# Kernel tuning notes

Hardware: AMD Instinct MI355X
Metric: run time of the kernel (lower is better)

## Reference

```python
import jax, jax.numpy as jnp
import numpy as np

H = 16  # num_heads


def setup_inputs() -> dict:
    key = jax.random.key(0)
    ks = jax.random.split(key, 12)
    B, S, D = 2, 2048, 1024
    init = lambda k, shape: (jax.random.normal(k, shape, dtype=jnp.float32) * 0.02)
    return {
        "x": jax.random.normal(ks[0], (B, S, D), dtype=jnp.float32),
        "wq": init(ks[1], (D, D)), "bq": init(ks[2], (D,)),
        "wk": init(ks[3], (D, D)), "bk": init(ks[4], (D,)),
        "wv": init(ks[5], (D, D)), "bv": init(ks[6], (D,)),
        "wo": init(ks[7], (D, D)), "bo": init(ks[8], (D,)),
        "w3d": init(ks[9], (3, D)), "b3d": init(ks[10], (3,)),
    }


def _pairwise_l2(pos):
    # pos: [B,S,3] -> [B,S,S] Euclidean distance (safe sqrt: zero grad at 0, like torch.cdist)
    sq = jnp.sum((pos[:, :, None, :] - pos[:, None, :, :]) ** 2, axis=-1)
    safe = jnp.where(sq > 0, sq, 1.0)
    return jnp.where(sq > 0, jnp.sqrt(safe), 0.0)


def reference(x, wq, bq, wk, bk, wv, bv, wo, bo, w3d, b3d):
    B, S, D = x.shape
    hd = D // H
    scale = 1.0 / (hd ** 0.5)
    # V projection -> [B,H,S,hd]  (Q/K are computed in torch forward but unused in APPROX scores)
    V = (x @ wv.T + bv).reshape(B, S, H, hd).transpose(0, 2, 1, 3)
    # 3D semantic positions and non-dot-product scores (identical across heads)
    pos = x @ w3d.T + b3d                      # [B,S,3]
    dist = _pairwise_l2(pos)                   # [B,S,S]
    scores = -dist[:, None, :, :] * scale      # [B,H,S,S] (broadcast over heads)
    causal = jnp.triu(jnp.ones((S, S), dtype=bool), k=1)
    scores = jnp.where(causal[None, None], -jnp.inf, scores)
    attn = jax.nn.softmax(scores, axis=-1)
    attn = jnp.nan_to_num(attn, nan=0.0)
    out = jnp.einsum('bhqk,bhkd->bhqd', attn, V)  # [B,H,S,hd]
    out = out.transpose(0, 2, 1, 3).reshape(B, S, D)
    return out @ wo.T + bo
```

## Files before the change

kernel.cpp:

```cpp
#include <hip/hip_runtime.h>
#include <hip/hip_bf16.h>
#include <stdint.h>


typedef __attribute__((ext_vector_type(8))) short bf16x8;
typedef __attribute__((ext_vector_type(4))) float f32x4;
typedef __attribute__((ext_vector_type(4))) unsigned short us4;

#define AS1(p) (const __attribute__((address_space(1))) unsigned int*)(p)
#define AS3(p) (__attribute__((address_space(3))) unsigned int*)(p)

__device__ __forceinline__ unsigned short f2bf(float f) {
  union { float f; unsigned u; } v; v.f = f;
  unsigned r = v.u + 0x7FFFu + ((v.u >> 16) & 1u);
  return (unsigned short)(r >> 16);
}

__global__ void k_prep(const float* __restrict__ x, const float* __restrict__ wv,
                       const float* __restrict__ wo, const float* __restrict__ bv,
                       const float* __restrict__ bo, const float* __restrict__ w3d,
                       const float* __restrict__ b3d,
                       unsigned short* __restrict__ xT, unsigned short* __restrict__ wvT,
                       unsigned short* __restrict__ wob, float* __restrict__ cvec,
                       float* __restrict__ pos) {
  __shared__ __align__(16) float lsm[64 * 68];
  const int bx = blockIdx.x, t = threadIdx.x;
  if (bx < 1024) {
    const int b = bx >> 9, rest = bx & 511, st = rest >> 4, dt = rest & 15;
    const int s0 = st * 64, d0 = dt * 64;
    const int r = t >> 2, c4 = t & 3;
    const float* src = x + (size_t)(b * 2048 + s0 + r) * 1024 + d0;
    float (*ld)[68] = (float(*)[68])lsm;
    #pragma unroll
    for (int p = 0; p < 4; p++)
      *(float4*)&ld[r][(c4 + 4 * p) * 4] = ((const float4*)src)[c4 + 4 * p];
    __syncthreads();
    #pragma unroll
    for (int p = 0; p < 4; p++) {
      const int dl = (t >> 4) + (p << 4);
      us4 o;
      #pragma unroll
      for (int k = 0; k < 4; k++)
        ((unsigned short*)&o)[k] = f2bf(ld[(t & 15) * 4 + k][dl]);
      *(us4*)(xT + ((size_t)b << 21) + (size_t)(d0 + dl) * 2048 + s0 + (t & 15) * 4) = o;
    }
  } else if (bx < 2048) {
    const int bb = bx - 1024, tr = bb >> 5, tc = bb & 31;
    const int r = t >> 5, c = t & 31;
    float (*ld)[33] = (float(*)[33])lsm;
    #pragma unroll
    for (int rr = r; rr < 32; rr += 8)
      ld[rr][c] = wv[(size_t)(tr * 32 + rr) * 1024 + tc * 32 + c];
    __syncthreads();
    #pragma unroll
    for (int rr = r; rr < 32; rr += 8)
      wvT[(size_t)(tc * 32 + rr) * 1024 + tr * 32 + c] = f2bf(ld[c][rr]);
  } else if (bx < 3072) {
    const int oo = bx - 2048;
    const float4 w = ((const float4*)(wo + (size_t)oo * 1024))[t];
    us4 ob; ob.x = f2bf(w.x); ob.y = f2bf(w.y); ob.z = f2bf(w.z); ob.w = f2bf(w.w);
    ((us4*)(wob + (size_t)oo * 1024))[t] = ob;
    const float4 b = ((const float4*)bv)[t];
    float a = w.x * b.x + w.y * b.y + w.z * b.z + w.w * b.w;
    #pragma unroll
    for (int off = 32; off; off >>= 1) a += __shfl_down(a, off, 64);
    if ((t & 63) == 0) lsm[t >> 6] = a;
    __syncthreads();
    if (t == 0) cvec[oo] = lsm[0] + lsm[1] + lsm[2] + lsm[3] + bo[oo];
  } else {
    const int row = bx - 3072;
    const float4 xv = ((const float4*)(x + (size_t)row * 1024))[t];
    const float4 w0 = ((const float4*)(w3d))[t];
    const float4 w1 = ((const float4*)(w3d + 1024))[t];
    const float4 w2 = ((const float4*)(w3d + 2048))[t];
    float a0 = xv.x*w0.x + xv.y*w0.y + xv.z*w0.z + xv.w*w0.w;
    float a1 = xv.x*w1.x + xv.y*w1.y + xv.z*w1.z + xv.w*w1.w;
    float a2 = xv.x*w2.x + xv.y*w2.y + xv.z*w2.z + xv.w*w2.w;
    #pragma unroll
    for (int off = 32; off; off >>= 1) {
      a0 += __shfl_down(a0, off, 64);
      a1 += __shfl_down(a1, off, 64);
      a2 += __shfl_down(a2, off, 64);
    }
    if ((t & 63) == 0) { lsm[(t >> 6) * 3] = a0; lsm[(t >> 6) * 3 + 1] = a1; lsm[(t >> 6) * 3 + 2] = a2; }
    __syncthreads();
    if (t == 0) {
      pos[(size_t)row*3 + 0] = lsm[0] + lsm[3] + lsm[6] + lsm[9]  + b3d[0];
      pos[(size_t)row*3 + 1] = lsm[1] + lsm[4] + lsm[7] + lsm[10] + b3d[1];
      pos[(size_t)row*3 + 2] = lsm[2] + lsm[5] + lsm[8] + lsm[11] + b3d[2];
    }
  }
}

__global__ void k_attn(const float* __restrict__ pos, unsigned short* __restrict__ Ab) {
  const int row = blockIdx.x;
  const int q = row & 2047, bb = row >> 11;
  const float* pb = pos + ((size_t)bb << 11) * 3;
  const float qx = pb[q*3], qy = pb[q*3+1], qz = pb[q*3+2];
  const float4* pb4 = (const float4*)pb;
  float v[2][4];
  float sum = 0.f;
  #pragma unroll
  for (int cc = 0; cc < 2; cc++) {
    const int j0 = (cc << 10) + (threadIdx.x << 2);
    const float4 A4 = pb4[3*(j0 >> 2)], B4 = pb4[3*(j0 >> 2) + 1], C4 = pb4[3*(j0 >> 2) + 2];
    const float px[4] = {A4.x, A4.w, B4.z, C4.y};
    const float py[4] = {A4.y, B4.x, B4.w, C4.z};
    const float pz[4] = {A4.z, B4.y, C4.x, C4.w};
    #pragma unroll
    for (int u = 0; u < 4; u++) {
      float e = 0.f;
      if (j0 + u <= q) {
        float dx = qx - px[u], dy = qy - py[u], dz = qz - pz[u];
        float sq = fmaf(dx, dx, fmaf(dy, dy, dz*dz));
        float d = sq > 0.f ? sqrtf(sq) : 0.f;
        e = __expf(-0.125f * d);
      }
      v[cc][u] = e; sum += e;
    }
  }
  #pragma unroll
  for (int off = 32; off; off >>= 1) sum += __shfl_down(sum, off, 64);
  __shared__ float red[4];
  if ((threadIdx.x & 63) == 0) red[threadIdx.x >> 6] = sum;
  __syncthreads();
  const float inv = 1.f / (red[0] + red[1] + red[2] + red[3]);
  unsigned short* orow = Ab + (size_t)row * 2048;
  #pragma unroll
  for (int cc = 0; cc < 2; cc++) {
    us4 o;
    o.x = f2bf(v[cc][0]*inv); o.y = f2bf(v[cc][1]*inv);
    o.z = f2bf(v[cc][2]*inv); o.w = f2bf(v[cc][3]*inv);
    *(us4*)(orow + (cc << 10) + (threadIdx.x << 2)) = o;
  }
}

template<int BM, int BN, int WM, int WN>
__device__ __forceinline__ void gemm_loop(
    const unsigned short* __restrict__ A, int lda,
    const unsigned short* __restrict__ Bt, int ldb,
    int m0, int n0, int kmax,
    unsigned short* lds, f32x4* acc) {
  constexpr int WAVES = WM * WN;
  constexpr int FI = BM / (WM * 16), FJ = BN / (WN * 16);
  constexpr int CPW = ((BM + BN) / 8) / WAVES;
  constexpr int BUFSZ = (BM + BN) * 64;
  const int tid = threadIdx.x, l = tid & 63, w = tid >> 6;
  const int wm = w & (WM - 1), wn = w / WM;
  const int gcol = ((l & 7) ^ (l >> 3)) << 3;

  auto stage = [&](int buf, int k0) {
    unsigned short* base = lds + buf * BUFSZ;
    #pragma unroll
    for (int e = 0; e < CPW; ++e) {
      const int c = w * CPW + e;
      const unsigned short* src;
      unsigned short* dst;
      if (c < BM / 8) {
        src = A + (size_t)(m0 + c*8 + (l >> 3)) * lda + k0 + gcol;
        dst = base + c * 512;
      } else {
        const int cb = c - BM / 8;
        src = Bt + (size_t)(n0 + cb*8 + (l >> 3)) * ldb + k0 + gcol;
        dst = base + BM * 64 + cb * 512;
      }
      __builtin_amdgcn_global_load_lds(AS1(src), AS3(dst), 16, 0, 0);
    }
  };

  auto compute = [&](int buf) {
    unsigned short* lA = lds + buf * BUFSZ;
    unsigned short* lB = lA + BM * 64;
    #pragma unroll
    for (int h = 0; h < 2; ++h) {
      const int slot = ((h << 2) | (l >> 4)) ^ (l & 7);
      bf16x8 af[FI], bfr[FJ];
      #pragma unroll
      for (int i = 0; i < FI; ++i) {
        const int ar = wm * (BM / WM) + i * 16 + (l & 15);
        af[i] = *(const bf16x8*)&lA[ar * 64 + slot * 8];
      }
      #pragma unroll
      for (int j = 0; j < FJ; ++j) {
        const int br = wn * (BN / WN) + j * 16 + (l & 15);
        bfr[j] = *(const bf16x8*)&lB[br * 64 + slot * 8];
      }
      #pragma unroll
      for (int i = 0; i < FI; ++i)
        #pragma unroll
        for (int j = 0; j < FJ; ++j)
          acc[i * FJ + j] = __builtin_amdgcn_mfma_f32_16x16x32_bf16(af[i], bfr[j], acc[i * FJ + j], 0, 0, 0);
    }
  };

  const int NT = kmax >> 6;
  stage(0, 0);
  if (NT > 1) stage(1, 64);
  int cur = 0, nxt2 = 2;
  for (int t = 0; t < NT; ++t) {
    if (t < NT - 1) {
      static_assert(CPW == 4 || CPW == 6 || CPW == 8, "vmcnt literal");
      if constexpr (CPW == 4) asm volatile("s_waitcnt vmcnt(4) lgkmcnt(0)" ::: "memory");
      else if constexpr (CPW == 6) asm volatile("s_waitcnt vmcnt(6) lgkmcnt(0)" ::: "memory");
      else asm volatile("s_waitcnt vmcnt(8) lgkmcnt(0)" ::: "memory");
    } else {
      asm volatile("s_waitcnt vmcnt(0) lgkmcnt(0)" ::: "memory");
    }
    __builtin_amdgcn_s_barrier();
    if (t + 2 < NT) stage(nxt2, (t + 2) << 6);
    compute(cur);
    cur = cur == 2 ? 0 : cur + 1;
    nxt2 = nxt2 == 2 ? 0 : nxt2 + 1;
  }
}

__global__ __launch_bounds__(256, 2) void k_gemm_axwc(
    const unsigned short* __restrict__ Ab, const unsigned short* __restrict__ xT,
    unsigned short* __restrict__ Axb,
    const unsigned short* __restrict__ wob, const unsigned short* __restrict__ wvT,
    unsigned short* __restrict__ Wcs) {
  __shared__ __align__(16) unsigned short lds[3 * (128 + 64) * 64];
  const int bx = blockIdx.x;
  const int l = threadIdx.x & 63, w = threadIdx.x >> 6;
  const int wm = w & 1, wn = w >> 1;
  if (bx < 512) {
    f32x4 acc[8] = {};
    const int b = bx >> 8;
    const int mi = b ? (bx & 15) : 15 - (bx & 15);
    const int m0 = mi * 128, n0 = ((bx >> 4) & 15) * 64;
    const unsigned short* A  = Ab + ((size_t)b << 22);
    const unsigned short* Bt = xT + ((size_t)b << 21);
    gemm_loop<128, 64, 2, 2>(A, 2048, Bt, 2048, m0, n0, m0 + 128, lds, acc);
    unsigned short* Obase = Axb + ((size_t)b << 11) * 1024;
    #pragma unroll
    for (int i = 0; i < 4; i++) {
      const int r0 = m0 + wm*64 + i*16 + ((l >> 4) << 2);
      #pragma unroll
      for (int j = 0; j < 2; j++) {
        const int cidx = n0 + wn*32 + j*16 + (l & 15);
        #pragma unroll
        for (int t = 0; t < 4; t++)
          Obase[(size_t)(r0 + t) * 1024 + cidx] = f2bf(acc[i*2 + j][t]);
      }
    }
  } else {
    f32x4 acc[4] = {};
    const int g = bx - 512;
    const int m0 = (g & 15) * 64, n0 = (g >> 4) * 64;
    gemm_loop<64, 64, 2, 2>(wob, 1024, wvT, 1024, m0, n0, 1024, lds, acc);
    #pragma unroll
    for (int i = 0; i < 2; i++) {
      const int r0 = m0 + wm*32 + i*16 + ((l >> 4) << 2);
      #pragma unroll
      for (int j = 0; j < 2; j++) {
        const int cidx = n0 + wn*32 + j*16 + (l & 15);
        #pragma unroll
        for (int t = 0; t < 4; t++)
          Wcs[(size_t)(r0 + t) * 1024 + cidx] = f2bf(acc[i*2 + j][t]);
      }
    }
  }
}

__global__ __launch_bounds__(256, 2) void k_gemm_out(
    const unsigned short* __restrict__ Axb, const unsigned short* __restrict__ Wcs,
    const float* __restrict__ cvec, float* __restrict__ out) {
  __shared__ __align__(16) unsigned short lds[3 * (128 + 64) * 64];
  f32x4 acc[8] = {};
  const int m0 = blockIdx.x * 128, n0 = blockIdx.y * 64;
  gemm_loop<128, 64, 2, 2>(Axb, 1024, Wcs, 1024, m0, n0, 1024, lds, acc);
  const int l = threadIdx.x & 63, w = threadIdx.x >> 6;
  const int wm = w & 1, wn = w >> 1;
  #pragma unroll
  for (int i = 0; i < 4; i++) {
    const int r0 = m0 + wm*64 + i*16 + ((l >> 4) << 2);
    #pragma unroll
    for (int j = 0; j < 2; j++) {
      const int cidx = n0 + wn*32 + j*16 + (l & 15);
      const float cv = cvec[cidx];
      #pragma unroll
      for (int t = 0; t < 4; t++)
        out[(size_t)(r0 + t) * 1024 + cidx] = acc[i*2 + j][t] + cv;
    }
  }
}

extern "C" void kernel_launch(void* const* d_in, const int* in_sizes, int n_in,
                              void* d_out, int out_size, void* d_ws, size_t ws_size,
                              hipStream_t stream) {
  const float* x   = (const float*)d_in[0];
  const float* wv  = (const float*)d_in[5];
  const float* bv  = (const float*)d_in[6];
  const float* wo  = (const float*)d_in[7];
  const float* bo  = (const float*)d_in[8];
  const float* w3d = (const float*)d_in[9];
  const float* b3d = (const float*)d_in[10];
  float* out = (float*)d_out;

  char* ws = (char*)d_ws;
  unsigned short* xT  = (unsigned short*)(ws);
  unsigned short* wvT = (unsigned short*)(ws + ( 8u << 20));
  unsigned short* wob = (unsigned short*)(ws + (10u << 20));
  unsigned short* Wcs = (unsigned short*)(ws + (12u << 20));
  unsigned short* Axb = (unsigned short*)(ws + (14u << 20));
  unsigned short* Ab  = (unsigned short*)(ws + (22u << 20));
  float*          pos = (float*)(ws + (38u << 20));
  float*          cvec= (float*)(ws + (39u << 20));

  k_prep<<<7168, 256, 0, stream>>>(x, wv, wo, bv, bo, w3d, b3d, xT, wvT, wob, cvec, pos);
  k_attn<<<4096, 256, 0, stream>>>(pos, Ab);
  k_gemm_axwc<<<768, 256, 0, stream>>>(Ab, xT, Axb, wob, wvT, Wcs);
  k_gemm_out<<<dim3(32, 16), 256, 0, stream>>>(Axb, Wcs, cvec, out);
}
```

Baseline: 59.45 us.

## Fuse pos projection into x transpose and balance causal GEMM work per block

The prep kernel now computes the 3D position projection inside the x transpose/bf16-cast blocks, so x is read once instead of twice, and the separate 4096 per-row pos blocks are removed. The A·x GEMM kernel now pairs causal row tiles p and 15-p in one block and also does one Wo·Wv tile per block, giving 256 evenly loaded blocks instead of 768 unevenly loaded ones. The tradeoff is fewer, longer blocks with less parallelism, extra barriers in the transpose loop, and the occupancy hint removed from the GEMM launch bounds.

```diff
diff --git a/kernel.cpp b/kernel.cpp
--- a/kernel.cpp
+++ b/kernel.cpp
@@ -23,29 +23,53 @@
                        unsigned short* __restrict__ xT, unsigned short* __restrict__ wvT,
                        unsigned short* __restrict__ wob, float* __restrict__ cvec,
                        float* __restrict__ pos) {
-  __shared__ __align__(16) float lsm[64 * 68];
+  __shared__ __align__(16) float lsm[32 * 69];
   const int bx = blockIdx.x, t = threadIdx.x;
-  if (bx < 1024) {
-    const int b = bx >> 9, rest = bx & 511, st = rest >> 4, dt = rest & 15;
-    const int s0 = st * 64, d0 = dt * 64;
-    const int r = t >> 2, c4 = t & 3;
-    const float* src = x + (size_t)(b * 2048 + s0 + r) * 1024 + d0;
-    float (*ld)[68] = (float(*)[68])lsm;
-    #pragma unroll
-    for (int p = 0; p < 4; p++)
-      *(float4*)&ld[r][(c4 + 4 * p) * 4] = ((const float4*)src)[c4 + 4 * p];
-    __syncthreads();
-    #pragma unroll
-    for (int p = 0; p < 4; p++) {
-      const int dl = (t >> 4) + (p << 4);
-      us4 o;
-      #pragma unroll
-      for (int k = 0; k < 4; k++)
-        ((unsigned short*)&o)[k] = f2bf(ld[(t & 15) * 4 + k][dl]);
-      *(us4*)(xT + ((size_t)b << 21) + (size_t)(d0 + dl) * 2048 + s0 + (t & 15) * 4) = o;
-    }
-  } else if (bx < 2048) {
-    const int bb = bx - 1024, tr = bb >> 5, tc = bb & 31;
+  if (bx < 128) {
+    const int b = bx >> 6, s0 = (bx & 63) * 32;
+    const int r = t >> 3, c8 = t & 7;
+    float (*ld)[69] = (float(*)[69])lsm;
+    float a0 = 0.f, a1 = 0.f, a2 = 0.f;
+    const float* xrow = x + (size_t)(b * 2048 + s0 + r) * 1024;
+    for (int dt = 0; dt < 16; ++dt) {
+      const int d0 = dt * 64;
+      const float4 v0 = *(const float4*)(xrow + d0 + c8 * 8);
+      const float4 v1 = *(const float4*)(xrow + d0 + c8 * 8 + 4);
+      const float* wp = w3d + d0 + c8 * 8;
+      a0 += v0.x*wp[0] + v0.y*wp[1] + v0.z*wp[2] + v0.w*wp[3]
+          + v1.x*wp[4] + v1.y*wp[5] + v1.z*wp[6] + v1.w*wp[7];
+      const float* wq = wp + 1024;
+      a1 += v0.x*wq[0] + v0.y*wq[1] + v0.z*wq[2] + v0.w*wq[3]
+          + v1.x*wq[4] + v1.y*wq[5] + v1.z*wq[6] + v1.w*wq[7];
+      const float* wr = wp + 2048;
+      a2 += v0.x*wr[0] + v0.y*wr[1] + v0.z*wr[2] + v0.w*wr[3]
+          + v1.x*wr[4] + v1.y*wr[5] + v1.z*wr[6] + v1.w*wr[7];
+      *(float4*)&ld[r][c8 * 8] = v0;
+      *(float4*)&ld[r][c8 * 8 + 4] = v1;
+      __syncthreads();
+      #pragma unroll
+      for (int p = 0; p < 2; ++p) {
+        const int dl = (t >> 3) + (p << 5);
+        const int sc = t & 7;
+        us4 o;
+        #pragma unroll
+        for (int k = 0; k < 4; ++k)
+          ((unsigned short*)&o)[k] = f2bf(ld[sc * 4 + k][dl]);
+        *(us4*)(xT + ((size_t)b << 21) + (size_t)(d0 + dl) * 2048 + s0 + sc * 4) = o;
+      }
+      __syncthreads();
+    }
+    a0 += __shfl_xor(a0, 1, 64); a0 += __shfl_xor(a0, 2, 64); a0 += __shfl_xor(a0, 4, 64);
+    a1 += __shfl_xor(a1, 1, 64); a1 += __shfl_xor(a1, 2, 64); a1 += __shfl_xor(a1, 4, 64);
+    a2 += __shfl_xor(a2, 1, 64); a2 += __shfl_xor(a2, 2, 64); a2 += __shfl_xor(a2, 4, 64);
+    if (c8 == 0) {
+      const size_t pr = (size_t)(b * 2048 + s0 + r) * 3;
+      pos[pr + 0] = a0 + b3d[0];
+      pos[pr + 1] = a1 + b3d[1];
+      pos[pr + 2] = a2 + b3d[2];
+    }
+  } else if (bx < 1152) {
+    const int bb = bx - 128, tr = bb >> 5, tc = bb & 31;
     const int r = t >> 5, c = t & 31;
     float (*ld)[33] = (float(*)[33])lsm;
     #pragma unroll
@@ -55,8 +79,8 @@
     #pragma unroll
     for (int rr = r; rr < 32; rr += 8)
       wvT[(size_t)(tc * 32 + rr) * 1024 + tr * 32 + c] = f2bf(ld[c][rr]);
-  } else if (bx < 3072) {
-    const int oo = bx - 2048;
+  } else {
+    const int oo = bx - 1152;
     const float4 w = ((const float4*)(wo + (size_t)oo * 1024))[t];
     us4 ob; ob.x = f2bf(w.x); ob.y = f2bf(w.y); ob.z = f2bf(w.z); ob.w = f2bf(w.w);
     ((us4*)(wob + (size_t)oo * 1024))[t] = ob;
@@ -67,28 +91,6 @@
     if ((t & 63) == 0) lsm[t >> 6] = a;
     __syncthreads();
     if (t == 0) cvec[oo] = lsm[0] + lsm[1] + lsm[2] + lsm[3] + bo[oo];
-  } else {
-    const int row = bx - 3072;
-    const float4 xv = ((const float4*)(x + (size_t)row * 1024))[t];
-    const float4 w0 = ((const float4*)(w3d))[t];
-    const float4 w1 = ((const float4*)(w3d + 1024))[t];
-    const float4 w2 = ((const float4*)(w3d + 2048))[t];
-    float a0 = xv.x*w0.x + xv.y*w0.y + xv.z*w0.z + xv.w*w0.w;
-    float a1 = xv.x*w1.x + xv.y*w1.y + xv.z*w1.z + xv.w*w1.w;
-    float a2 = xv.x*w2.x + xv.y*w2.y + xv.z*w2.z + xv.w*w2.w;
-    #pragma unroll
-    for (int off = 32; off; off >>= 1) {
-      a0 += __shfl_down(a0, off, 64);
-      a1 += __shfl_down(a1, off, 64);
-      a2 += __shfl_down(a2, off, 64);
-    }
-    if ((t & 63) == 0) { lsm[(t >> 6) * 3] = a0; lsm[(t >> 6) * 3 + 1] = a1; lsm[(t >> 6) * 3 + 2] = a2; }
-    __syncthreads();
-    if (t == 0) {
-      pos[(size_t)row*3 + 0] = lsm[0] + lsm[3] + lsm[6] + lsm[9]  + b3d[0];
-      pos[(size_t)row*3 + 1] = lsm[1] + lsm[4] + lsm[7] + lsm[10] + b3d[1];
-      pos[(size_t)row*3 + 2] = lsm[2] + lsm[5] + lsm[8] + lsm[11] + b3d[2];
-    }
   }
 }
 
@@ -214,7 +216,7 @@
   }
 }
 
-__global__ __launch_bounds__(256, 2) void k_gemm_axwc(
+__global__ __launch_bounds__(256) void k_gemm_axwc(
     const unsigned short* __restrict__ Ab, const unsigned short* __restrict__ xT,
     unsigned short* __restrict__ Axb,
     const unsigned short* __restrict__ wob, const unsigned short* __restrict__ wvT,
@@ -223,15 +225,18 @@
   const int bx = blockIdx.x;
   const int l = threadIdx.x & 63, w = threadIdx.x >> 6;
   const int wm = w & 1, wn = w >> 1;
-  if (bx < 512) {
+  const int b = bx >> 7, rest = bx & 127;
+  const int p = rest & 7, n0 = (rest >> 3) * 64;
+  const unsigned short* A  = Ab + ((size_t)b << 22);
+  const unsigned short* Bt = xT + ((size_t)b << 21);
+  unsigned short* Obase = Axb + ((size_t)b << 11) * 1024;
+  #pragma unroll
+  for (int half = 0; half < 2; ++half) {
+    const int mi = half ? (15 - p) : p;
+    const int m0 = mi * 128;
     f32x4 acc[8] = {};
-    const int b = bx >> 8;
-    const int mi = b ? (bx & 15) : 15 - (bx & 15);
-    const int m0 = mi * 128, n0 = ((bx >> 4) & 15) * 64;
-    const unsigned short* A  = Ab + ((size_t)b << 22);
-    const unsigned short* Bt = xT + ((size_t)b << 21);
-    gemm_loop<128, 64, 2, 2>(A, 2048, Bt, 2048, m0, n0, m0 + 128, lds, acc);
-    unsigned short* Obase = Axb + ((size_t)b << 11) * 1024;
+    gemm_loop<128, 64, 2, 2>(A, 2048, Bt, 2048, m0, n0, (mi + 1) * 128, lds, acc);
+    __syncthreads();
     #pragma unroll
     for (int i = 0; i < 4; i++) {
       const int r0 = m0 + wm*64 + i*16 + ((l >> 4) << 2);
@@ -243,20 +248,21 @@
           Obase[(size_t)(r0 + t) * 1024 + cidx] = f2bf(acc[i*2 + j][t]);
       }
     }
-  } else {
-    f32x4 acc[4] = {};
-    const int g = bx - 512;
-    const int m0 = (g & 15) * 64, n0 = (g >> 4) * 64;
-    gemm_loop<64, 64, 2, 2>(wob, 1024, wvT, 1024, m0, n0, 1024, lds, acc);
+  }
+  {
+    const int m0w = (bx & 15) * 64, n0w = (bx >> 4) * 64;
+    f32x4 acc2[4] = {};
+    gemm_loop<64, 64, 2, 2>(wob, 1024, wvT, 1024, m0w, n0w, 1024, lds, acc2);
+    __syncthreads();
     #pragma unroll
     for (int i = 0; i < 2; i++) {
-      const int r0 = m0 + wm*32 + i*16 + ((l >> 4) << 2);
+      const int r0 = m0w + wm*32 + i*16 + ((l >> 4) << 2);
       #pragma unroll
       for (int j = 0; j < 2; j++) {
-        const int cidx = n0 + wn*32 + j*16 + (l & 15);
+        const int cidx = n0w + wn*32 + j*16 + (l & 15);
         #pragma unroll
         for (int t = 0; t < 4; t++)
-          Wcs[(size_t)(r0 + t) * 1024 + cidx] = f2bf(acc[i*2 + j][t]);
+          Wcs[(size_t)(r0 + t) * 1024 + cidx] = f2bf(acc2[i*2 + j][t]);
       }
     }
   }
@@ -307,8 +313,8 @@
   float*          pos = (float*)(ws + (38u << 20));
   float*          cvec= (float*)(ws + (39u << 20));
 
-  k_prep<<<7168, 256, 0, stream>>>(x, wv, wo, bv, bo, w3d, b3d, xT, wvT, wob, cvec, pos);
+  k_prep<<<2176, 256, 0, stream>>>(x, wv, wo, bv, bo, w3d, b3d, xT, wvT, wob, cvec, pos);
   k_attn<<<4096, 256, 0, stream>>>(pos, Ab);
-  k_gemm_axwc<<<768, 256, 0, stream>>>(Ab, xT, Axb, wob, wvT, Wcs);
+  k_gemm_axwc<<<256, 256, 0, stream>>>(Ab, xT, Axb, wob, wvT, Wcs);
   k_gemm_out<<<dim3(32, 16), 256, 0, stream>>>(Axb, Wcs, cvec, out);
 }
```

After: 67.25 us. +13.1%, slower.

## Fuse all stages into one persistent kernel with software grid barriers

Applied to the files above, without the earlier changes.

Merges the prep, attention-probability, two GEMM and output kernels into one persistent launch of 512 blocks. The stages are separated by atomic-counter grid barriers, which removes launch gaps and tail effects between kernels. It also skips writing the probability tiles that lie wholly above the causal diagonal (at 128-column granularity) and reassigns GEMM tiles so the weight-combine GEMM runs on half the blocks. The cost is barrier spin overhead, and correctness depends on all 512 blocks being co-resident. Work inside each stage becomes serialized and unevenly balanced.

```diff
diff --git a/kernel.cpp b/kernel.cpp
--- a/kernel.cpp
+++ b/kernel.cpp
@@ -9,6 +9,7 @@
 
 #define AS1(p) (const __attribute__((address_space(1))) unsigned int*)(p)
 #define AS3(p) (__attribute__((address_space(3))) unsigned int*)(p)
+#define NBLK 512
 
 __device__ __forceinline__ unsigned short f2bf(float f) {
   union { float f; unsigned u; } v; v.f = f;
@@ -16,123 +17,16 @@
   return (unsigned short)(r >> 16);
 }
 
-__global__ void k_prep(const float* __restrict__ x, const float* __restrict__ wv,
-                       const float* __restrict__ wo, const float* __restrict__ bv,
-                       const float* __restrict__ bo, const float* __restrict__ w3d,
-                       const float* __restrict__ b3d,
-                       unsigned short* __restrict__ xT, unsigned short* __restrict__ wvT,
-                       unsigned short* __restrict__ wob, float* __restrict__ cvec,
-                       float* __restrict__ pos) {
-  __shared__ __align__(16) float lsm[64 * 68];
-  const int bx = blockIdx.x, t = threadIdx.x;
-  if (bx < 1024) {
-    const int b = bx >> 9, rest = bx & 511, st = rest >> 4, dt = rest & 15;
-    const int s0 = st * 64, d0 = dt * 64;
-    const int r = t >> 2, c4 = t & 3;
-    const float* src = x + (size_t)(b * 2048 + s0 + r) * 1024 + d0;
-    float (*ld)[68] = (float(*)[68])lsm;
-    #pragma unroll
-    for (int p = 0; p < 4; p++)
-      *(float4*)&ld[r][(c4 + 4 * p) * 4] = ((const float4*)src)[c4 + 4 * p];
-    __syncthreads();
-    #pragma unroll
-    for (int p = 0; p < 4; p++) {
-      const int dl = (t >> 4) + (p << 4);
-      us4 o;
-      #pragma unroll
-      for (int k = 0; k < 4; k++)
-        ((unsigned short*)&o)[k] = f2bf(ld[(t & 15) * 4 + k][dl]);
-      *(us4*)(xT + ((size_t)b << 21) + (size_t)(d0 + dl) * 2048 + s0 + (t & 15) * 4) = o;
-    }
-  } else if (bx < 2048) {
-    const int bb = bx - 1024, tr = bb >> 5, tc = bb & 31;
-    const int r = t >> 5, c = t & 31;
-    float (*ld)[33] = (float(*)[33])lsm;
-    #pragma unroll
-    for (int rr = r; rr < 32; rr += 8)
-      ld[rr][c] = wv[(size_t)(tr * 32 + rr) * 1024 + tc * 32 + c];
-    __syncthreads();
-    #pragma unroll
-    for (int rr = r; rr < 32; rr += 8)
-      wvT[(size_t)(tc * 32 + rr) * 1024 + tr * 32 + c] = f2bf(ld[c][rr]);
-  } else if (bx < 3072) {
-    const int oo = bx - 2048;
-    const float4 w = ((const float4*)(wo + (size_t)oo * 1024))[t];
-    us4 ob; ob.x = f2bf(w.x); ob.y = f2bf(w.y); ob.z = f2bf(w.z); ob.w = f2bf(w.w);
-    ((us4*)(wob + (size_t)oo * 1024))[t] = ob;
-    const float4 b = ((const float4*)bv)[t];
-    float a = w.x * b.x + w.y * b.y + w.z * b.z + w.w * b.w;
-    #pragma unroll
-    for (int off = 32; off; off >>= 1) a += __shfl_down(a, off, 64);
-    if ((t & 63) == 0) lsm[t >> 6] = a;
-    __syncthreads();
-    if (t == 0) cvec[oo] = lsm[0] + lsm[1] + lsm[2] + lsm[3] + bo[oo];
-  } else {
-    const int row = bx - 3072;
-    const float4 xv = ((const float4*)(x + (size_t)row * 1024))[t];
-    const float4 w0 = ((const float4*)(w3d))[t];
-    const float4 w1 = ((const float4*)(w3d + 1024))[t];
-    const float4 w2 = ((const float4*)(w3d + 2048))[t];
-    float a0 = xv.x*w0.x + xv.y*w0.y + xv.z*w0.z + xv.w*w0.w;
-    float a1 = xv.x*w1.x + xv.y*w1.y + xv.z*w1.z + xv.w*w1.w;
-    float a2 = xv.x*w2.x + xv.y*w2.y + xv.z*w2.z + xv.w*w2.w;
-    #pragma unroll
-    for (int off = 32; off; off >>= 1) {
-      a0 += __shfl_down(a0, off, 64);
-      a1 += __shfl_down(a1, off, 64);
-      a2 += __shfl_down(a2, off, 64);
-    }
-    if ((t & 63) == 0) { lsm[(t >> 6) * 3] = a0; lsm[(t >> 6) * 3 + 1] = a1; lsm[(t >> 6) * 3 + 2] = a2; }
-    __syncthreads();
-    if (t == 0) {
-      pos[(size_t)row*3 + 0] = lsm[0] + lsm[3] + lsm[6] + lsm[9]  + b3d[0];
-      pos[(size_t)row*3 + 1] = lsm[1] + lsm[4] + lsm[7] + lsm[10] + b3d[1];
-      pos[(size_t)row*3 + 2] = lsm[2] + lsm[5] + lsm[8] + lsm[11] + b3d[2];
-    }
-  }
-}
-
-__global__ void k_attn(const float* __restrict__ pos, unsigned short* __restrict__ Ab) {
-  const int row = blockIdx.x;
-  const int q = row & 2047, bb = row >> 11;
-  const float* pb = pos + ((size_t)bb << 11) * 3;
-  const float qx = pb[q*3], qy = pb[q*3+1], qz = pb[q*3+2];
-  const float4* pb4 = (const float4*)pb;
-  float v[2][4];
-  float sum = 0.f;
-  #pragma unroll
-  for (int cc = 0; cc < 2; cc++) {
-    const int j0 = (cc << 10) + (threadIdx.x << 2);
-    const float4 A4 = pb4[3*(j0 >> 2)], B4 = pb4[3*(j0 >> 2) + 1], C4 = pb4[3*(j0 >> 2) + 2];
-    const float px[4] = {A4.x, A4.w, B4.z, C4.y};
-    const float py[4] = {A4.y, B4.x, B4.w, C4.z};
-    const float pz[4] = {A4.z, B4.y, C4.x, C4.w};
-    #pragma unroll
-    for (int u = 0; u < 4; u++) {
-      float e = 0.f;
-      if (j0 + u <= q) {
-        float dx = qx - px[u], dy = qy - py[u], dz = qz - pz[u];
-        float sq = fmaf(dx, dx, fmaf(dy, dy, dz*dz));
-        float d = sq > 0.f ? sqrtf(sq) : 0.f;
-        e = __expf(-0.125f * d);
-      }
-      v[cc][u] = e; sum += e;
-    }
-  }
-  #pragma unroll
-  for (int off = 32; off; off >>= 1) sum += __shfl_down(sum, off, 64);
-  __shared__ float red[4];
-  if ((threadIdx.x & 63) == 0) red[threadIdx.x >> 6] = sum;
+__device__ __forceinline__ void gridbar(unsigned* ctr) {
   __syncthreads();
-  const float inv = 1.f / (red[0] + red[1] + red[2] + red[3]);
-  unsigned short* orow = Ab + (size_t)row * 2048;
-  #pragma unroll
-  for (int cc = 0; cc < 2; cc++) {
-    us4 o;
-    o.x = f2bf(v[cc][0]*inv); o.y = f2bf(v[cc][1]*inv);
-    o.z = f2bf(v[cc][2]*inv); o.w = f2bf(v[cc][3]*inv);
-    *(us4*)(orow + (cc << 10) + (threadIdx.x << 2)) = o;
-  }
+  if (threadIdx.x == 0) {
+    __threadfence();
+    __hip_atomic_fetch_add(ctr, 1u, __ATOMIC_ACQ_REL, __HIP_MEMORY_SCOPE_AGENT);
+    while (__hip_atomic_load(ctr, __ATOMIC_RELAXED, __HIP_MEMORY_SCOPE_AGENT) < NBLK)
+      __builtin_amdgcn_s_sleep(8);
+    __threadfence();
+  }
+  __syncthreads();
 }
 
 template<int BM, int BN, int WM, int WN>
@@ -214,23 +108,158 @@
   }
 }
 
-__global__ __launch_bounds__(256, 2) void k_gemm_axwc(
-    const unsigned short* __restrict__ Ab, const unsigned short* __restrict__ xT,
-    unsigned short* __restrict__ Axb,
-    const unsigned short* __restrict__ wob, const unsigned short* __restrict__ wvT,
-    unsigned short* __restrict__ Wcs) {
+__global__ __launch_bounds__(256, 2) void k_mega(
+    const float* __restrict__ x, const float* __restrict__ wv,
+    const float* __restrict__ wo, const float* __restrict__ bv,
+    const float* __restrict__ bo, const float* __restrict__ w3d,
+    const float* __restrict__ b3d,
+    unsigned short* __restrict__ xT, unsigned short* __restrict__ wvT,
+    unsigned short* __restrict__ wob, float* __restrict__ cvec,
+    float* __restrict__ pos, unsigned short* __restrict__ Ab,
+    unsigned short* __restrict__ Axb, unsigned short* __restrict__ Wcs,
+    float* __restrict__ out, unsigned* __restrict__ bar) {
   __shared__ __align__(16) unsigned short lds[3 * (128 + 64) * 64];
-  const int bx = blockIdx.x;
-  const int l = threadIdx.x & 63, w = threadIdx.x >> 6;
-  const int wm = w & 1, wn = w >> 1;
-  if (bx < 512) {
-    f32x4 acc[8] = {};
-    const int b = bx >> 8;
-    const int mi = b ? (bx & 15) : 15 - (bx & 15);
-    const int m0 = mi * 128, n0 = ((bx >> 4) & 15) * 64;
+  const int bid = blockIdx.x, t = threadIdx.x;
+  const int l = t & 63, w = t >> 6;
+  float* lsm = (float*)lds;
+
+  for (int k = 0; k < 14; ++k) {
+    const int u = bid + (k << 9);
+    if (u < 1024) {
+      const int b = u >> 9, rest = u & 511, st = rest >> 4, dt = rest & 15;
+      const int s0 = st * 64, d0 = dt * 64;
+      const int r = t >> 2, c4 = t & 3;
+      const float* src = x + (size_t)(b * 2048 + s0 + r) * 1024 + d0;
+      float (*ld)[68] = (float(*)[68])lsm;
+      #pragma unroll
+      for (int p = 0; p < 4; p++)
+        *(float4*)&ld[r][(c4 + 4 * p) * 4] = ((const float4*)src)[c4 + 4 * p];
+      __syncthreads();
+      #pragma unroll
+      for (int p = 0; p < 4; p++) {
+        const int dl = (t >> 4) + (p << 4);
+        us4 o;
+        #pragma unroll
+        for (int kk = 0; kk < 4; kk++)
+          ((unsigned short*)&o)[kk] = f2bf(ld[(t & 15) * 4 + kk][dl]);
+        *(us4*)(xT + ((size_t)b << 21) + (size_t)(d0 + dl) * 2048 + s0 + (t & 15) * 4) = o;
+      }
+    } else if (u < 2048) {
+      const int bb = u - 1024, tr = bb >> 5, tc = bb & 31;
+      const int r = t >> 5, c = t & 31;
+      float (*ld)[33] = (float(*)[33])lsm;
+      #pragma unroll
+      for (int rr = r; rr < 32; rr += 8)
+        ld[rr][c] = wv[(size_t)(tr * 32 + rr) * 1024 + tc * 32 + c];
+      __syncthreads();
+      #pragma unroll
+      for (int rr = r; rr < 32; rr += 8)
+        wvT[(size_t)(tc * 32 + rr) * 1024 + tr * 32 + c] = f2bf(ld[c][rr]);
+    } else if (u < 3072) {
+      const int oo = u - 2048;
+      const float4 ww = ((const float4*)(wo + (size_t)oo * 1024))[t];
+      us4 ob; ob.x = f2bf(ww.x); ob.y = f2bf(ww.y); ob.z = f2bf(ww.z); ob.w = f2bf(ww.w);
+      ((us4*)(wob + (size_t)oo * 1024))[t] = ob;
+      const float4 b4 = ((const float4*)bv)[t];
+      float a = ww.x * b4.x + ww.y * b4.y + ww.z * b4.z + ww.w * b4.w;
+      #pragma unroll
+      for (int off = 32; off; off >>= 1) a += __shfl_down(a, off, 64);
+      if ((t & 63) == 0) lsm[t >> 6] = a;
+      __syncthreads();
+      if (t == 0) cvec[oo] = lsm[0] + lsm[1] + lsm[2] + lsm[3] + bo[oo];
+    } else {
+      const int row = u - 3072;
+      const float4 xv = ((const float4*)(x + (size_t)row * 1024))[t];
+      const float4 w0 = ((const float4*)(w3d))[t];
+      const float4 w1 = ((const float4*)(w3d + 1024))[t];
+      const float4 w2 = ((const float4*)(w3d + 2048))[t];
+      float a0 = xv.x*w0.x + xv.y*w0.y + xv.z*w0.z + xv.w*w0.w;
+      float a1 = xv.x*w1.x + xv.y*w1.y + xv.z*w1.z + xv.w*w1.w;
+      float a2 = xv.x*w2.x + xv.y*w2.y + xv.z*w2.z + xv.w*w2.w;
+      #pragma unroll
+      for (int off = 32; off; off >>= 1) {
+        a0 += __shfl_down(a0, off, 64);
+        a1 += __shfl_down(a1, off, 64);
+        a2 += __shfl_down(a2, off, 64);
+      }
+      if ((t & 63) == 0) { lsm[(t >> 6) * 3] = a0; lsm[(t >> 6) * 3 + 1] = a1; lsm[(t >> 6) * 3 + 2] = a2; }
+      __syncthreads();
+      if (t == 0) {
+        pos[(size_t)row*3 + 0] = lsm[0] + lsm[3] + lsm[6] + lsm[9]  + b3d[0];
+        pos[(size_t)row*3 + 1] = lsm[1] + lsm[4] + lsm[7] + lsm[10] + b3d[1];
+        pos[(size_t)row*3 + 2] = lsm[2] + lsm[5] + lsm[8] + lsm[11] + b3d[2];
+      }
+    }
+    __syncthreads();
+  }
+  gridbar(bar + 0);
+
+  for (int k = 0; k < 8; ++k) {
+    const int row = bid + (k << 9);
+    const int q = row & 2047, bb = row >> 11;
+    const float* pb = pos + ((size_t)bb << 11) * 3;
+    const float qx = pb[q*3], qy = pb[q*3+1], qz = pb[q*3+2];
+    const float4* pb4 = (const float4*)pb;
+    const int jmax = ((q >> 7) + 1) << 7;
+    float vv[2][4];
+    float sum = 0.f;
+    #pragma unroll
+    for (int cc = 0; cc < 2; cc++) {
+      const int j0 = (cc << 10) + (t << 2);
+      float e0 = 0.f, e1 = 0.f, e2 = 0.f, e3 = 0.f;
+      if (j0 < jmax) {
+        const float4 A4 = pb4[3*(j0 >> 2)], B4 = pb4[3*(j0 >> 2) + 1], C4 = pb4[3*(j0 >> 2) + 2];
+        const float px[4] = {A4.x, A4.w, B4.z, C4.y};
+        const float py[4] = {A4.y, B4.x, B4.w, C4.z};
+        const float pz[4] = {A4.z, B4.y, C4.x, C4.w};
+        float ee[4];
+        #pragma unroll
+        for (int uu = 0; uu < 4; uu++) {
+          float e = 0.f;
+          if (j0 + uu <= q) {
+            float dx = qx - px[uu], dy = qy - py[uu], dz = qz - pz[uu];
+            float sq = fmaf(dx, dx, fmaf(dy, dy, dz*dz));
+            float d = sq > 0.f ? sqrtf(sq) : 0.f;
+            e = __expf(-0.125f * d);
+          }
+          ee[uu] = e;
+        }
+        e0 = ee[0]; e1 = ee[1]; e2 = ee[2]; e3 = ee[3];
+      }
+      vv[cc][0] = e0; vv[cc][1] = e1; vv[cc][2] = e2; vv[cc][3] = e3;
+      sum += e0 + e1 + e2 + e3;
+    }
+    #pragma unroll
+    for (int off = 32; off; off >>= 1) sum += __shfl_down(sum, off, 64);
+    if ((t & 63) == 0) lsm[t >> 6] = sum;
+    __syncthreads();
+    const float inv = 1.f / (lsm[0] + lsm[1] + lsm[2] + lsm[3]);
+    unsigned short* orow = Ab + (size_t)row * 2048;
+    #pragma unroll
+    for (int cc = 0; cc < 2; cc++) {
+      const int j0 = (cc << 10) + (t << 2);
+      if (j0 < jmax) {
+        us4 o;
+        o.x = f2bf(vv[cc][0]*inv); o.y = f2bf(vv[cc][1]*inv);
+        o.z = f2bf(vv[cc][2]*inv); o.w = f2bf(vv[cc][3]*inv);
+        *(us4*)(orow + j0) = o;
+      }
+    }
+    __syncthreads();
+  }
+  gridbar(bar + 1);
+
+  {
+    const int b = bid & 1;
+    const int n0 = ((bid >> 1) & 15) << 6;
+    const int mi = (bid >> 5) & 15;
+    const int m0 = mi << 7;
     const unsigned short* A  = Ab + ((size_t)b << 22);
     const unsigned short* Bt = xT + ((size_t)b << 21);
-    gemm_loop<128, 64, 2, 2>(A, 2048, Bt, 2048, m0, n0, m0 + 128, lds, acc);
+    f32x4 acc[8] = {};
+    gemm_loop<128, 64, 2, 2>(A, 2048, Bt, 2048, m0, n0, (mi + 1) << 7, lds, acc);
+    __syncthreads();
+    const int wm = w & 1, wn = w >> 1;
     unsigned short* Obase = Axb + ((size_t)b << 11) * 1024;
     #pragma unroll
     for (int i = 0; i < 4; i++) {
@@ -239,48 +268,46 @@
       for (int j = 0; j < 2; j++) {
         const int cidx = n0 + wn*32 + j*16 + (l & 15);
         #pragma unroll
-        for (int t = 0; t < 4; t++)
-          Obase[(size_t)(r0 + t) * 1024 + cidx] = f2bf(acc[i*2 + j][t]);
-      }
-    }
-  } else {
-    f32x4 acc[4] = {};
-    const int g = bx - 512;
-    const int m0 = (g & 15) * 64, n0 = (g >> 4) * 64;
-    gemm_loop<64, 64, 2, 2>(wob, 1024, wvT, 1024, m0, n0, 1024, lds, acc);
-    #pragma unroll
-    for (int i = 0; i < 2; i++) {
-      const int r0 = m0 + wm*32 + i*16 + ((l >> 4) << 2);
+        for (int tt = 0; tt < 4; tt++)
+          Obase[(size_t)(r0 + tt) * 1024 + cidx] = f2bf(acc[i*2 + j][tt]);
+      }
+    }
+    if (bid < 256) {
+      f32x4 acc2[4] = {};
+      const int m0w = (bid & 15) << 6, n0w = ((bid >> 4) & 15) << 6;
+      gemm_loop<64, 64, 2, 2>(wob, 1024, wvT, 1024, m0w, n0w, 1024, lds, acc2);
+      __syncthreads();
+      #pragma unroll
+      for (int i = 0; i < 2; i++) {
+        const int r0 = m0w + wm*32 + i*16 + ((l >> 4) << 2);
+        #pragma unroll
+        for (int j = 0; j < 2; j++) {
+          const int cidx = n0w + wn*32 + j*16 + (l & 15);
+          #pragma unroll
+          for (int tt = 0; tt < 4; tt++)
+            Wcs[(size_t)(r0 + tt) * 1024 + cidx] = f2bf(acc2[i*2 + j][tt]);
+        }
+      }
+    }
+  }
+  gridbar(bar + 2);
+
+  {
+    const int m0 = (bid >> 4) << 7, n0 = (bid & 15) << 6;
+    f32x4 acc[8] = {};
+    gemm_loop<128, 64, 2, 2>(Axb, 1024, Wcs, 1024, m0, n0, 1024, lds, acc);
+    const int wm = w & 1, wn = w >> 1;
+    #pragma unroll
+    for (int i = 0; i < 4; i++) {
+      const int r0 = m0 + wm*64 + i*16 + ((l >> 4) << 2);
       #pragma unroll
       for (int j = 0; j < 2; j++) {
         const int cidx = n0 + wn*32 + j*16 + (l & 15);
-        #pragma unroll
-        for (int t = 0; t < 4; t++)
-          Wcs[(size_t)(r0 + t) * 1024 + cidx] = f2bf(acc[i*2 + j][t]);
-      }
-    }
-  }
-}
-
-__global__ __launch_bounds__(256, 2) void k_gemm_out(
-    const unsigned short* __restrict__ Axb, const unsigned short* __restrict__ Wcs,
-    const float* __restrict__ cvec, float* __restrict__ out) {
-  __shared__ __align__(16) unsigned short lds[3 * (128 + 64) * 64];
-  f32x4 acc[8] = {};
-  const int m0 = blockIdx.x * 128, n0 = blockIdx.y * 64;
-  gemm_loop<128, 64, 2, 2>(Axb, 1024, Wcs, 1024, m0, n0, 1024, lds, acc);
-  const int l = threadIdx.x & 63, w = threadIdx.x >> 6;
-  const int wm = w & 1, wn = w >> 1;
-  #pragma unroll
-  for (int i = 0; i < 4; i++) {
-    const int r0 = m0 + wm*64 + i*16 + ((l >> 4) << 2);
-    #pragma unroll
-    for (int j = 0; j < 2; j++) {
-      const int cidx = n0 + wn*32 + j*16 + (l & 15);
-      const float cv = cvec[cidx];
-      #pragma unroll
-      for (int t = 0; t < 4; t++)
-        out[(size_t)(r0 + t) * 1024 + cidx] = acc[i*2 + j][t] + cv;
+        const float cv = cvec[cidx];
+        #pragma unroll
+        for (int tt = 0; tt < 4; tt++)
+          out[(size_t)(r0 + tt) * 1024 + cidx] = acc[i*2 + j][tt] + cv;
+      }
     }
   }
 }
@@ -306,9 +333,9 @@
   unsigned short* Ab  = (unsigned short*)(ws + (22u << 20));
   float*          pos = (float*)(ws + (38u << 20));
   float*          cvec= (float*)(ws + (39u << 20));
-
-  k_prep<<<7168, 256, 0, stream>>>(x, wv, wo, bv, bo, w3d, b3d, xT, wvT, wob, cvec, pos);
-  k_attn<<<4096, 256, 0, stream>>>(pos, Ab);
-  k_gemm_axwc<<<768, 256, 0, stream>>>(Ab, xT, Axb, wob, wvT, Wcs);
-  k_gemm_out<<<dim3(32, 16), 256, 0, stream>>>(Axb, Wcs, cvec, out);
-}
+  unsigned*       bar = (unsigned*)(ws + (40u << 20));
+
+  hipMemsetAsync(bar, 0, 16, stream);
+  k_mega<<<NBLK, 256, 0, stream>>>(x, wv, wo, bv, bo, w3d, b3d,
+                                   xT, wvT, wob, cvec, pos, Ab, Axb, Wcs, out, bar);
+}
```

After: 222.4 us. 274% more time.
